# Kernel tuning notes

Hardware: AMD Instinct MI355X
Metric: run time of the kernel (lower is better)

## Reference

```python
import jax, jax.numpy as jnp
import numpy as np
from jax.scipy.special import logsumexp

B, D, T, O = 8, 64, 512, 256  # batch, channels (d_dim), observed timestamps, grid points


def setup_inputs() -> dict:
    key = jax.random.key(0)
    k1, k2, k3 = jax.random.split(key, 3)
    vals = jax.random.normal(k1, (B, D, T), dtype=jnp.float32)
    mask = (jax.random.uniform(k2, (B, D, T)) < 0.7).astype(jnp.float32)
    mask = mask.at[:, :, 0].set(1.0)  # ensure >=1 observation per (b, channel)
    times = jnp.sort(jax.random.uniform(k3, (B, D, T), dtype=jnp.float32), axis=-1)
    x = jnp.concatenate([vals, mask, times], axis=1)  # (B, 3*D, T)
    grid = jnp.broadcast_to(jnp.linspace(0.0, 1.0, O, dtype=jnp.float32), (B, O))
    kernel = jnp.zeros((D,), dtype=jnp.float32)  # learned per-channel log-bandwidth
    return {"x": x, "interpolation_grid": grid, "kernel": kernel}


def reference(x, interpolation_grid, kernel):
    d_dim = kernel.shape[0]
    x_t = x[:, :d_dim]            # (B, D, T) observed values
    m = x[:, d_dim:2 * d_dim]     # (B, D, T) observation mask in {0,1}
    t = x[:, 2 * d_dim:3 * d_dim] # (B, D, T) observation timestamps

    alpha = jax.nn.softplus(kernel)[None, :, None, None]  # pos_kernel, (1,D,1,1)
    # squared distance between observed times and reference grid: (B,D,T,O)
    norm = (t[:, :, :, None] - interpolation_grid[:, None, None, :]) ** 2
    # log(mask): -inf (clamped) where unobserved, 0 where observed
    logm = jnp.log(jnp.maximum(m, 1e-30))[:, :, :, None]

    s = -alpha * norm + logm                      # (B,D,T,O) masked RBF logits
    w = logsumexp(s, axis=2)                      # (B,D,O) intensity channel
    w1 = jnp.exp(s - w[:, :, None, :])            # softmax over T
    y = jnp.sum(w1 * x_t[:, :, :, None], axis=2)  # (B,D,O) smooth interpolation

    s10 = -10.0 * alpha * norm + logm             # sharper kernel (transient)
    wt_lse = logsumexp(s10, axis=2)
    wt = jnp.exp(s10 - wt_lse[:, :, None, :])
    y_trans = jnp.sum(wt * x_t[:, :, :, None], axis=2)  # (B,D,O)

    return jnp.concatenate([y, w, y_trans], axis=1)  # (B, 3*D, O)
```

## Files before the change

### kernel.cpp

```cpp
#include <hip/hip_runtime.h>
#include <math.h>


namespace {
constexpr int kB = 8, kD = 64, kT = 512, kO = 256;
constexpr float kLOG2E = 1.4426950408889634f;
constexpr float kLN2   = 0.6931471805599453f;
}

__global__ __launch_bounds__(kO) void interp_kernel(
    const float* __restrict__ x,
    const float* __restrict__ grid,
    const float* __restrict__ kern,
    float* __restrict__ out)
{
    __shared__ __align__(16) float s_t[kT];
    __shared__ __align__(16) float s_lm[kT];
    __shared__ __align__(16) float s_v[kT];

    const int bd = blockIdx.x;
    const int b  = bd >> 6;
    const int d  = bd & (kD - 1);
    const int o  = threadIdx.x;

    const float* base  = x + (size_t)b * (3 * kD * kT);
    const float* vals  = base + (size_t)d * kT;
    const float* mask  = base + (size_t)(kD + d) * kT;
    const float* times = base + (size_t)(2 * kD + d) * kT;

    for (int i = o; i < kT; i += kO) {
        s_v[i]  = vals[i];
        s_t[i]  = times[i];
        s_lm[i] = __builtin_amdgcn_logf(fmaxf(mask[i], 1e-30f));
    }
    __syncthreads();

    const float k     = kern[d];
    const float alpha = fmaxf(k, 0.0f) + log1pf(expf(-fabsf(k)));
    const float a2    = alpha * kLOG2E;
    const float a10   = 10.0f * a2;
    const float g     = grid[b * kO + o];

    float l0=0.f,l1=0.f,l2=0.f,l3=0.f;
    float y0=0.f,y1=0.f,y2=0.f,y3=0.f;
    float q0=0.f,q1=0.f,q2=0.f,q3=0.f;
    float z0=0.f,z1=0.f,z2=0.f,z3=0.f;

    #pragma unroll 2
    for (int t = 0; t < kT; t += 4) {
        const float4 tt = *(const float4*)(s_t  + t);
        const float4 lm = *(const float4*)(s_lm + t);
        const float4 vv = *(const float4*)(s_v  + t);

        { float dd = tt.x - g; float nn = dd * dd;
          float p = __builtin_amdgcn_exp2f(fmaf(-a2,  nn, lm.x));
          float r = __builtin_amdgcn_exp2f(fmaf(-a10, nn, lm.x));
          l0 += p; y0 = fmaf(p, vv.x, y0);
          q0 += r; z0 = fmaf(r, vv.x, z0); }
        { float dd = tt.y - g; float nn = dd * dd;
          float p = __builtin_amdgcn_exp2f(fmaf(-a2,  nn, lm.y));
          float r = __builtin_amdgcn_exp2f(fmaf(-a10, nn, lm.y));
          l1 += p; y1 = fmaf(p, vv.y, y1);
          q1 += r; z1 = fmaf(r, vv.y, z1); }
        { float dd = tt.z - g; float nn = dd * dd;
          float p = __builtin_amdgcn_exp2f(fmaf(-a2,  nn, lm.z));
          float r = __builtin_amdgcn_exp2f(fmaf(-a10, nn, lm.z));
          l2 += p; y2 = fmaf(p, vv.z, y2);
          q2 += r; z2 = fmaf(r, vv.z, z2); }
        { float dd = tt.w - g; float nn = dd * dd;
          float p = __builtin_amdgcn_exp2f(fmaf(-a2,  nn, lm.w));
          float r = __builtin_amdgcn_exp2f(fmaf(-a10, nn, lm.w));
          l3 += p; y3 = fmaf(p, vv.w, y3);
          q3 += r; z3 = fmaf(r, vv.w, z3); }
    }

    const float l  = (l0 + l1) + (l2 + l3);
    const float ya = (y0 + y1) + (y2 + y3);
    const float q  = (q0 + q1) + (q2 + q3);
    const float za = (z0 + z1) + (z2 + z3);

    const float w = __builtin_amdgcn_logf(l) * kLN2;

    float* ob = out + (size_t)b * (3 * kD * kO);
    ob[(size_t)d * kO + o]            = ya / l;
    ob[(size_t)(kD + d) * kO + o]     = w;
    ob[(size_t)(2 * kD + d) * kO + o] = za / q;
}

extern "C" void kernel_launch(void* const* d_in, const int* in_sizes, int n_in,
                              void* d_out, int out_size, void* d_ws, size_t ws_size,
                              hipStream_t stream) {
    const float* x    = (const float*)d_in[0];
    const float* grid = (const float*)d_in[1];
    const float* kern = (const float*)d_in[2];
    float* out        = (float*)d_out;
    interp_kernel<<<dim3(kB * kD), dim3(kO), 0, stream>>>(x, grid, kern, out);
}
```

Baseline: 79.12 us.

## Split T across four thread groups and derive sharp kernel by squaring

Each block now has 1024 threads: four groups each cover a quarter of the timestamps, and their partial sums are combined through shared memory before one group writes the output. The exponent is expanded as u + w*g + c, with per-timestamp terms precomputed once during the load. The sharp-kernel weight is obtained as e^10 through repeated squaring instead of a second exp2. The goal is higher occupancy on a grid of only 512 blocks and about half the transcendental work. The costs are an extra barrier and reduction, and some loss of precision from expanding the squared distance.

```diff
diff --git a/kernel.cpp b/kernel.cpp
--- a/kernel.cpp
+++ b/kernel.cpp
@@ -4,87 +4,110 @@
 
 namespace {
 constexpr int kB = 8, kD = 64, kT = 512, kO = 256;
+constexpr int kQ = 4;
+constexpr int kTH = kO * kQ;
+constexpr int kTQ = kT / kQ;
 constexpr float kLOG2E = 1.4426950408889634f;
 constexpr float kLN2   = 0.6931471805599453f;
 }
 
-__global__ __launch_bounds__(kO) void interp_kernel(
+__global__ __launch_bounds__(kTH, 8) void interp_kernel(
     const float* __restrict__ x,
     const float* __restrict__ grid,
     const float* __restrict__ kern,
     float* __restrict__ out)
 {
-    __shared__ __align__(16) float s_t[kT];
-    __shared__ __align__(16) float s_lm[kT];
-    __shared__ __align__(16) float s_v[kT];
+    __shared__ __align__(16) float smem[4096];
+    float* s_u = smem;
+    float* s_w = smem + kT;
+    float* s_v = smem + 2 * kT;
 
-    const int bd = blockIdx.x;
-    const int b  = bd >> 6;
-    const int d  = bd & (kD - 1);
-    const int o  = threadIdx.x;
+    const int tid = threadIdx.x;
+    const int o   = tid & (kO - 1);
+    const int q   = tid >> 8;
+    const int bd  = blockIdx.x;
+    const int b   = bd >> 6;
+    const int d   = bd & (kD - 1);
 
     const float* base  = x + (size_t)b * (3 * kD * kT);
     const float* vals  = base + (size_t)d * kT;
     const float* mask  = base + (size_t)(kD + d) * kT;
     const float* times = base + (size_t)(2 * kD + d) * kT;
 
-    for (int i = o; i < kT; i += kO) {
-        s_v[i]  = vals[i];
-        s_t[i]  = times[i];
-        s_lm[i] = __builtin_amdgcn_logf(fmaxf(mask[i], 1e-30f));
+    const float k     = kern[d];
+    const float alpha = fmaxf(k, 0.0f) + log1pf(expf(-fabsf(k)));
+    const float a2    = alpha * kLOG2E;
+
+    if (tid < kT) {
+        const float tt = times[tid];
+        const float mm = mask[tid];
+        const float lm = __builtin_amdgcn_logf(fmaxf(mm, 1e-30f));
+        s_u[tid] = fmaf(-a2 * tt, tt, lm);
+        s_w[tid] = 2.0f * a2 * tt;
+        s_v[tid] = vals[tid];
     }
     __syncthreads();
 
-    const float k     = kern[d];
-    const float alpha = fmaxf(k, 0.0f) + log1pf(expf(-fabsf(k)));
-    const float a2    = alpha * kLOG2E;
-    const float a10   = 10.0f * a2;
-    const float g     = grid[b * kO + o];
+    const float g = grid[b * kO + o];
+    const float c = -a2 * g * g;
 
     float l0=0.f,l1=0.f,l2=0.f,l3=0.f;
     float y0=0.f,y1=0.f,y2=0.f,y3=0.f;
     float q0=0.f,q1=0.f,q2=0.f,q3=0.f;
     float z0=0.f,z1=0.f,z2=0.f,z3=0.f;
 
+    const int t0 = q * kTQ;
     #pragma unroll 2
-    for (int t = 0; t < kT; t += 4) {
-        const float4 tt = *(const float4*)(s_t  + t);
-        const float4 lm = *(const float4*)(s_lm + t);
-        const float4 vv = *(const float4*)(s_v  + t);
+    for (int t = t0; t < t0 + kTQ; t += 4) {
+        const float4 uu = *(const float4*)(s_u + t);
+        const float4 ww = *(const float4*)(s_w + t);
+        const float4 vv = *(const float4*)(s_v + t);
 
-        { float dd = tt.x - g; float nn = dd * dd;
-          float p = __builtin_amdgcn_exp2f(fmaf(-a2,  nn, lm.x));
-          float r = __builtin_amdgcn_exp2f(fmaf(-a10, nn, lm.x));
-          l0 += p; y0 = fmaf(p, vv.x, y0);
-          q0 += r; z0 = fmaf(r, vv.x, z0); }
-        { float dd = tt.y - g; float nn = dd * dd;
-          float p = __builtin_amdgcn_exp2f(fmaf(-a2,  nn, lm.y));
-          float r = __builtin_amdgcn_exp2f(fmaf(-a10, nn, lm.y));
-          l1 += p; y1 = fmaf(p, vv.y, y1);
-          q1 += r; z1 = fmaf(r, vv.y, z1); }
-        { float dd = tt.z - g; float nn = dd * dd;
-          float p = __builtin_amdgcn_exp2f(fmaf(-a2,  nn, lm.z));
-          float r = __builtin_amdgcn_exp2f(fmaf(-a10, nn, lm.z));
-          l2 += p; y2 = fmaf(p, vv.z, y2);
-          q2 += r; z2 = fmaf(r, vv.z, z2); }
-        { float dd = tt.w - g; float nn = dd * dd;
-          float p = __builtin_amdgcn_exp2f(fmaf(-a2,  nn, lm.w));
-          float r = __builtin_amdgcn_exp2f(fmaf(-a10, nn, lm.w));
-          l3 += p; y3 = fmaf(p, vv.w, y3);
-          q3 += r; z3 = fmaf(r, vv.w, z3); }
+        { float e1 = __builtin_amdgcn_exp2f(fmaf(ww.x, g, uu.x) + c);
+          float e2 = e1*e1, e4 = e2*e2, e8 = e4*e4, r = e8*e2;
+          l0 += e1; y0 = fmaf(e1, vv.x, y0);
+          q0 += r;  z0 = fmaf(r,  vv.x, z0); }
+        { float e1 = __builtin_amdgcn_exp2f(fmaf(ww.y, g, uu.y) + c);
+          float e2 = e1*e1, e4 = e2*e2, e8 = e4*e4, r = e8*e2;
+          l1 += e1; y1 = fmaf(e1, vv.y, y1);
+          q1 += r;  z1 = fmaf(r,  vv.y, z1); }
+        { float e1 = __builtin_amdgcn_exp2f(fmaf(ww.z, g, uu.z) + c);
+          float e2 = e1*e1, e4 = e2*e2, e8 = e4*e4, r = e8*e2;
+          l2 += e1; y2 = fmaf(e1, vv.z, y2);
+          q2 += r;  z2 = fmaf(r,  vv.z, z2); }
+        { float e1 = __builtin_amdgcn_exp2f(fmaf(ww.w, g, uu.w) + c);
+          float e2 = e1*e1, e4 = e2*e2, e8 = e4*e4, r = e8*e2;
+          l3 += e1; y3 = fmaf(e1, vv.w, y3);
+          q3 += r;  z3 = fmaf(r,  vv.w, z3); }
     }
 
-    const float l  = (l0 + l1) + (l2 + l3);
-    const float ya = (y0 + y1) + (y2 + y3);
-    const float q  = (q0 + q1) + (q2 + q3);
-    const float za = (z0 + z1) + (z2 + z3);
+    const float lp = (l0 + l1) + (l2 + l3);
+    const float yp = (y0 + y1) + (y2 + y3);
+    const float qp = (q0 + q1) + (q2 + q3);
+    const float zp = (z0 + z1) + (z2 + z3);
 
-    const float w = __builtin_amdgcn_logf(l) * kLN2;
+    __syncthreads();
+    smem[(q * 4 + 0) * kO + o] = lp;
+    smem[(q * 4 + 1) * kO + o] = yp;
+    smem[(q * 4 + 2) * kO + o] = qp;
+    smem[(q * 4 + 3) * kO + o] = zp;
+    __syncthreads();
 
-    float* ob = out + (size_t)b * (3 * kD * kO);
-    ob[(size_t)d * kO + o]            = ya / l;
-    ob[(size_t)(kD + d) * kO + o]     = w;
-    ob[(size_t)(2 * kD + d) * kO + o] = za / q;
+    if (q == 0) {
+        float l = 0.f, ya = 0.f, qs = 0.f, za = 0.f;
+        #pragma unroll
+        for (int j = 0; j < kQ; ++j) {
+            l  += smem[(j * 4 + 0) * kO + o];
+            ya += smem[(j * 4 + 1) * kO + o];
+            qs += smem[(j * 4 + 2) * kO + o];
+            za += smem[(j * 4 + 3) * kO + o];
+        }
+        const float w = __builtin_amdgcn_logf(l) * kLN2;
+        float* ob = out + (size_t)b * (3 * kD * kO);
+        ob[(size_t)d * kO + o]            = ya / l;
+        ob[(size_t)(kD + d) * kO + o]     = w;
+        ob[(size_t)(2 * kD + d) * kO + o] = za / qs;
+    }
 }
 
 extern "C" void kernel_launch(void* const* d_in, const int* in_sizes, int n_in,
@@ -94,5 +117,5 @@
     const float* grid = (const float*)d_in[1];
     const float* kern = (const float*)d_in[2];
     float* out        = (float*)d_out;
-    interp_kernel<<<dim3(kB * kD), dim3(kO), 0, stream>>>(x, grid, kern, out);
+    interp_kernel<<<dim3(kB * kD), dim3(kTH), 0, stream>>>(x, grid, kern, out);
 }
```

Result: faster. 77.01 us (-2.7%).

## Expand squared distance algebraically, broadcast samples via readlane, split T across waves

Applied to the files above, without the earlier changes.

Rewrites the exponent -a(t-g)^2 + log m as a per-sample affine function of g. The per-grid -a·g^2 term cancels in both softmax ratios, so it is dropped from the loop and added back only for the log-intensity output. The sharp kernel reuses the same exponent scaled by 10. Per-sample coefficients are broadcast across the wavefront with readlane instead of being read from LDS. The block grows to 512 threads: each wave covers 128 timestamps for two grid points, and partials are reduced through shared memory. This cuts VALU work per exp pair and removes LDS traffic in the hot loop, at the cost of a reduction step and a possibly larger rounding error in the expanded form.

```diff
diff --git a/kernel.cpp b/kernel.cpp
--- a/kernel.cpp
+++ b/kernel.cpp
@@ -6,85 +6,106 @@
 constexpr int kB = 8, kD = 64, kT = 512, kO = 256;
 constexpr float kLOG2E = 1.4426950408889634f;
 constexpr float kLN2   = 0.6931471805599453f;
+constexpr int kTH = 512;
 }
 
-__global__ __launch_bounds__(kO) void interp_kernel(
+__device__ __forceinline__ float rlane(float v, int l) {
+    return __int_as_float(__builtin_amdgcn_readlane(__float_as_int(v), l));
+}
+
+__global__ __launch_bounds__(kTH, 4) void interp_kernel(
     const float* __restrict__ x,
     const float* __restrict__ grid,
     const float* __restrict__ kern,
     float* __restrict__ out)
 {
-    __shared__ __align__(16) float s_t[kT];
-    __shared__ __align__(16) float s_lm[kT];
-    __shared__ __align__(16) float s_v[kT];
+    __shared__ float sp[4][4][kO];
+
+    const int tid  = threadIdx.x;
+    const int lane = tid & 63;
+    const int wv   = tid >> 6;
+    const int ow   = wv & 1;
+    const int tw   = wv >> 1;
+    const int o0   = ow * 128 + lane;
+    const int t0   = tw * 128;
 
     const int bd = blockIdx.x;
     const int b  = bd >> 6;
     const int d  = bd & (kD - 1);
-    const int o  = threadIdx.x;
 
-    const float* base  = x + (size_t)b * (3 * kD * kT);
-    const float* vals  = base + (size_t)d * kT;
-    const float* mask  = base + (size_t)(kD + d) * kT;
-    const float* times = base + (size_t)(2 * kD + d) * kT;
-
-    for (int i = o; i < kT; i += kO) {
-        s_v[i]  = vals[i];
-        s_t[i]  = times[i];
-        s_lm[i] = __builtin_amdgcn_logf(fmaxf(mask[i], 1e-30f));
-    }
-    __syncthreads();
+    const float* base = x + (size_t)b * (3 * kD * kT);
+    const float* Vrow = base + (size_t)d * kT;
+    const float* Mrow = base + (size_t)(kD + d) * kT;
+    const float* Trow = base + (size_t)(2 * kD + d) * kT;
 
     const float k     = kern[d];
     const float alpha = fmaxf(k, 0.0f) + log1pf(expf(-fabsf(k)));
     const float a2    = alpha * kLOG2E;
-    const float a10   = 10.0f * a2;
-    const float g     = grid[b * kO + o];
 
-    float l0=0.f,l1=0.f,l2=0.f,l3=0.f;
-    float y0=0.f,y1=0.f,y2=0.f,y3=0.f;
-    float q0=0.f,q1=0.f,q2=0.f,q3=0.f;
-    float z0=0.f,z1=0.f,z2=0.f,z3=0.f;
+    const float tt0 = Trow[t0 + lane],      tt1 = Trow[t0 + 64 + lane];
+    const float mm0 = Mrow[t0 + lane],      mm1 = Mrow[t0 + 64 + lane];
+    const float vv0 = Vrow[t0 + lane],      vv1 = Vrow[t0 + 64 + lane];
+    const float lm0 = __builtin_amdgcn_logf(fmaxf(mm0, 1e-30f));
+    const float lm1 = __builtin_amdgcn_logf(fmaxf(mm1, 1e-30f));
+    const float u0  = fmaf(-a2 * tt0, tt0, lm0);
+    const float u1  = fmaf(-a2 * tt1, tt1, lm1);
+    const float w0  = 2.0f * a2 * tt0;
+    const float w1  = 2.0f * a2 * tt1;
 
-    #pragma unroll 2
-    for (int t = 0; t < kT; t += 4) {
-        const float4 tt = *(const float4*)(s_t  + t);
-        const float4 lm = *(const float4*)(s_lm + t);
-        const float4 vv = *(const float4*)(s_v  + t);
+    const float g0 = grid[b * kO + o0];
+    const float g1 = grid[b * kO + o0 + 64];
 
-        { float dd = tt.x - g; float nn = dd * dd;
-          float p = __builtin_amdgcn_exp2f(fmaf(-a2,  nn, lm.x));
-          float r = __builtin_amdgcn_exp2f(fmaf(-a10, nn, lm.x));
-          l0 += p; y0 = fmaf(p, vv.x, y0);
-          q0 += r; z0 = fmaf(r, vv.x, z0); }
-        { float dd = tt.y - g; float nn = dd * dd;
-          float p = __builtin_amdgcn_exp2f(fmaf(-a2,  nn, lm.y));
-          float r = __builtin_amdgcn_exp2f(fmaf(-a10, nn, lm.y));
-          l1 += p; y1 = fmaf(p, vv.y, y1);
-          q1 += r; z1 = fmaf(r, vv.y, z1); }
-        { float dd = tt.z - g; float nn = dd * dd;
-          float p = __builtin_amdgcn_exp2f(fmaf(-a2,  nn, lm.z));
-          float r = __builtin_amdgcn_exp2f(fmaf(-a10, nn, lm.z));
-          l2 += p; y2 = fmaf(p, vv.z, y2);
-          q2 += r; z2 = fmaf(r, vv.z, z2); }
-        { float dd = tt.w - g; float nn = dd * dd;
-          float p = __builtin_amdgcn_exp2f(fmaf(-a2,  nn, lm.w));
-          float r = __builtin_amdgcn_exp2f(fmaf(-a10, nn, lm.w));
-          l3 += p; y3 = fmaf(p, vv.w, y3);
-          q3 += r; z3 = fmaf(r, vv.w, z3); }
+    float l_0=0.f,l_1=0.f, y_0=0.f,y_1=0.f, q_0=0.f,q_1=0.f, z_0=0.f,z_1=0.f;
+
+    #pragma unroll
+    for (int j = 0; j < 64; ++j) {
+        { const float us = rlane(u0, j), ws = rlane(w0, j), vs = rlane(vv0, j);
+          const float a0 = ws * g0 + us;
+          const float a1 = ws * g1 + us;
+          const float e0 = __builtin_amdgcn_exp2f(a0);
+          const float E0 = __builtin_amdgcn_exp2f(10.0f * a0);
+          const float e1 = __builtin_amdgcn_exp2f(a1);
+          const float E1 = __builtin_amdgcn_exp2f(10.0f * a1);
+          l_0 += e0; y_0 = fmaf(e0, vs, y_0); q_0 += E0; z_0 = fmaf(E0, vs, z_0);
+          l_1 += e1; y_1 = fmaf(e1, vs, y_1); q_1 += E1; z_1 = fmaf(E1, vs, z_1); }
+        { const float us = rlane(u1, j), ws = rlane(w1, j), vs = rlane(vv1, j);
+          const float a0 = ws * g0 + us;
+          const float a1 = ws * g1 + us;
+          const float e0 = __builtin_amdgcn_exp2f(a0);
+          const float E0 = __builtin_amdgcn_exp2f(10.0f * a0);
+          const float e1 = __builtin_amdgcn_exp2f(a1);
+          const float E1 = __builtin_amdgcn_exp2f(10.0f * a1);
+          l_0 += e0; y_0 = fmaf(e0, vs, y_0); q_0 += E0; z_0 = fmaf(E0, vs, z_0);
+          l_1 += e1; y_1 = fmaf(e1, vs, y_1); q_1 += E1; z_1 = fmaf(E1, vs, z_1); }
     }
 
-    const float l  = (l0 + l1) + (l2 + l3);
-    const float ya = (y0 + y1) + (y2 + y3);
-    const float q  = (q0 + q1) + (q2 + q3);
-    const float za = (z0 + z1) + (z2 + z3);
+    sp[tw][0][o0] = l_0;  sp[tw][0][o0 + 64] = l_1;
+    sp[tw][1][o0] = y_0;  sp[tw][1][o0 + 64] = y_1;
+    sp[tw][2][o0] = q_0;  sp[tw][2][o0 + 64] = q_1;
+    sp[tw][3][o0] = z_0;  sp[tw][3][o0 + 64] = z_1;
+    __syncthreads();
 
-    const float w = __builtin_amdgcn_logf(l) * kLN2;
-
-    float* ob = out + (size_t)b * (3 * kD * kO);
-    ob[(size_t)d * kO + o]            = ya / l;
-    ob[(size_t)(kD + d) * kO + o]     = w;
-    ob[(size_t)(2 * kD + d) * kO + o] = za / q;
+    if (tw == 0) {
+        float L0=0.f,L1=0.f, Y0=0.f,Y1=0.f, Q0=0.f,Q1=0.f, Z0=0.f,Z1=0.f;
+        #pragma unroll
+        for (int j = 0; j < 4; ++j) {
+            L0 += sp[j][0][o0]; Y0 += sp[j][1][o0];
+            Q0 += sp[j][2][o0]; Z0 += sp[j][3][o0];
+            L1 += sp[j][0][o0 + 64]; Y1 += sp[j][1][o0 + 64];
+            Q1 += sp[j][2][o0 + 64]; Z1 += sp[j][3][o0 + 64];
+        }
+        const float c0 = -a2 * g0 * g0;
+        const float c1 = -a2 * g1 * g1;
+        const float w0o = (__builtin_amdgcn_logf(L0) + c0) * kLN2;
+        const float w1o = (__builtin_amdgcn_logf(L1) + c1) * kLN2;
+        float* ob = out + (size_t)b * (3 * kD * kO);
+        ob[(size_t)d * kO + o0]                 = Y0 / L0;
+        ob[(size_t)d * kO + o0 + 64]            = Y1 / L1;
+        ob[(size_t)(kD + d) * kO + o0]          = w0o;
+        ob[(size_t)(kD + d) * kO + o0 + 64]     = w1o;
+        ob[(size_t)(2 * kD + d) * kO + o0]      = Z0 / Q0;
+        ob[(size_t)(2 * kD + d) * kO + o0 + 64] = Z1 / Q1;
+    }
 }
 
 extern "C" void kernel_launch(void* const* d_in, const int* in_sizes, int n_in,
@@ -94,5 +115,5 @@
     const float* grid = (const float*)d_in[1];
     const float* kern = (const float*)d_in[2];
     float* out        = (float*)d_out;
-    interp_kernel<<<dim3(kB * kD), dim3(kO), 0, stream>>>(x, grid, kern, out);
+    interp_kernel<<<dim3(kB * kD), dim3(kTH), 0, stream>>>(x, grid, kern, out);
 }
```

New measurement: 80.14 us. No clear change (+1.3%).
